# Kernel tuning notes

Measured on AMD Instinct MI355X. Metric: run time of the kernel, lower is better.

Reference implementation:

```python
import jax, jax.numpy as jnp
import numpy as np

B = 256      # graph pairs
N = 256      # nodes per graph (uniform -> padding is a reshape)
DEG = 16     # avg degree
D = 32       # one_hot_dim
F1, F2, F3 = 128, 64, 64
T = 16       # tensor_neurons
BINS = 16
BOT = 16     # bottle_neck_neurons


def setup_inputs() -> dict:
    key = jax.random.key(0)
    ks = jax.random.split(key, 24)
    NT = B * N            # total nodes per side
    NE = B * N * DEG      # total directed edges per side
    x_q = jax.random.normal(ks[0], (NT, D), jnp.float32)
    x_c = jax.random.normal(ks[1], (NT, D), jnp.float32)
    edge_q = jax.random.randint(ks[2], (2, NE), 0, NT, jnp.int32)
    edge_c = jax.random.randint(ks[3], (2, NE), 0, NT, jnp.int32)
    qgraph_sizes = jnp.full((B,), N, jnp.int32)
    cgraph_sizes = jnp.full((B,), N, jnp.int32)

    def glorot(k, shape):
        fan = sum(shape[-2:]) if len(shape) >= 2 else shape[0] * 2
        return jax.random.uniform(k, shape, jnp.float32, -1.0, 1.0) * np.sqrt(6.0 / fan)

    params = dict(
        W1=glorot(ks[4], (D, F1)), b1=jnp.zeros((F1,), jnp.float32),
        W2=glorot(ks[5], (F1, F2)), b2=jnp.zeros((F2,), jnp.float32),
        W3=glorot(ks[6], (F2, F3)), b3=jnp.zeros((F3,), jnp.float32),
        attn_w=glorot(ks[7], (F3, F3)),
        ntn_a_w=glorot(ks[8], (T, F3, F3)),
        ntn_b_w=glorot(ks[9], (2 * F3, T)),
        ntn_bias=glorot(ks[10], (T, 1)),
        fc1_w=glorot(ks[11], (T + BINS, BOT)), fc1_b=jnp.zeros((BOT,), jnp.float32),
        fc2_w=glorot(ks[12], (BOT, 1)), fc2_b=jnp.zeros((1,), jnp.float32),
    )
    return dict(x_q=x_q, edge_q=edge_q, x_c=x_c, edge_c=edge_c,
                qgraph_sizes=qgraph_sizes, cgraph_sizes=cgraph_sizes, **params)


def _gcn(x, src, dst, W, b):
    n = x.shape[0]
    h = x @ W
    loop = jnp.arange(n, dtype=src.dtype)
    s = jnp.concatenate([src, loop])
    d = jnp.concatenate([dst, loop])
    deg = jax.ops.segment_sum(jnp.ones(s.shape, h.dtype), d, num_segments=n)
    dinv = jnp.where(deg > 0, jax.lax.rsqrt(jnp.maximum(deg, 1.0)), 0.0)
    coef = (dinv[s] * dinv[d])[:, None]
    return jax.ops.segment_sum(h[s] * coef, d, num_segments=n) + b


def _gnn(x, ei, W1, b1, W2, b2, W3, b3):
    src, dst = ei[0], ei[1]
    h = jax.nn.relu(_gcn(x, src, dst, W1, b1))        # dropout is identity in eval
    h = jax.nn.relu(_gcn(h, src, dst, W2, b2))
    return _gcn(h, src, dst, W3, b3)                  # [B*N, F3]


def _att_pool(q, attn_w, sizes):
    # q: [B, N, F3]
    ctx = jnp.tanh((q.sum(axis=1) @ attn_w) / sizes.astype(q.dtype)[:, None])  # [B, F3]
    sig = jax.nn.sigmoid(jnp.einsum('bnf,bf->bn', q, ctx))                      # [B, N]
    return jnp.einsum('bnf,bn->bf', q, sig)                                     # [B, F3]


def _pair_hist(q, c):
    # per-pair histogram of q @ c^T with BINS bins over each pair's [min, max]
    s = jax.lax.stop_gradient(jnp.einsum('bnf,bmf->bnm', q, c))  # [B, N, N]
    mn = s.min(axis=(1, 2), keepdims=True)
    mx = s.max(axis=(1, 2), keepdims=True)
    idx = jnp.clip(jnp.floor((s - mn) / jnp.maximum(mx - mn, 1e-12) * BINS),
                   0, BINS - 1).astype(jnp.int32)
    gid = (idx + jnp.arange(B, dtype=jnp.int32)[:, None, None] * BINS).reshape(-1)
    h = jax.ops.segment_sum(jnp.ones(gid.shape, jnp.float32), gid,
                            num_segments=B * BINS).reshape(B, BINS)
    return h / h.sum(axis=1, keepdims=True)


def reference(x_q, edge_q, x_c, edge_c, qgraph_sizes, cgraph_sizes,
              W1, b1, W2, b2, W3, b3, attn_w, ntn_a_w, ntn_b_w, ntn_bias,
              fc1_w, fc1_b, fc2_w, fc2_b):
    q = _gnn(x_q, edge_q, W1, b1, W2, b2, W3, b3).reshape(B, N, F3)
    c = _gnn(x_c, edge_c, W1, b1, W2, b2, W3, b3).reshape(B, N, F3)
    e1 = _att_pool(q, attn_w, qgraph_sizes)
    e2 = _att_pool(c, attn_w, cgraph_sizes)
    ntn = (jnp.einsum('bi,tij,bj->bt', e1, ntn_a_w, e2)
           + jnp.concatenate([e1, e2], axis=-1) @ ntn_b_w
           + ntn_bias[:, 0])
    scores = jax.nn.relu(ntn)                                   # [B, T]
    hist = _pair_hist(q, c)                                     # [B, BINS]
    scores = jnp.concatenate([scores, hist], axis=1)
    scores = jax.nn.relu(scores @ fc1_w + fc1_b)
    p = jax.nn.sigmoid(scores @ fc2_w + fc2_b)[:, 0]            # [B]
    ged = -0.5 * (qgraph_sizes + cgraph_sizes).astype(p.dtype) * jnp.log(p)
    return ged
```

## Files before the change

kernel.cpp:

```cpp
#include <hip/hip_runtime.h>
#include <hip/hip_bf16.h>
#include <math.h>

#define BB 256
#define NN 256
#define NT (BB*NN)
#define NT2 (2*NT)
#define NE (NT*16)
#define DD 32
#define F1C 128
#define F2C 64
#define F3C 64
#define TT 16
#define BINS 16

#define NBUCK 256
#define BSHIFT 9
#define BNODES 512
#define BCAP 10240
#define EPB 4096

typedef __attribute__((ext_vector_type(8))) short short8;
typedef __attribute__((ext_vector_type(4))) float f32x4;
typedef __attribute__((ext_vector_type(2))) float f32x2;

__device__ inline float b2f(ushort u) { return __uint_as_float(((uint)u) << 16); }
__device__ inline ushort f2b(float f) {
    uint u = __float_as_uint(f);
    return (ushort)((u + 0x7fffu + ((u >> 16) & 1u)) >> 16);
}
__device__ inline float clamp8(float v) { return fminf(fmaxf(v, -448.0f), 448.0f); }
__device__ inline uchar f2f8(float v) {
    int r = __builtin_amdgcn_cvt_pk_fp8_f32(clamp8(v), 0.0f, 0, false);
    return (uchar)(r & 0xff);
}
__device__ inline void f8x8_acc(uint2 w, float* acc) {
    f32x2 p;
    p = __builtin_amdgcn_cvt_pk_f32_fp8(w.x, false); acc[0] += p.x; acc[1] += p.y;
    p = __builtin_amdgcn_cvt_pk_f32_fp8(w.x, true);  acc[2] += p.x; acc[3] += p.y;
    p = __builtin_amdgcn_cvt_pk_f32_fp8(w.y, false); acc[4] += p.x; acc[5] += p.y;
    p = __builtin_amdgcn_cvt_pk_f32_fp8(w.y, true);  acc[6] += p.x; acc[7] += p.y;
}
__device__ inline uint2 f8x8_pack(const float* v) {
    uint2 r;
    r.x = (uint)__builtin_amdgcn_cvt_pk_fp8_f32(clamp8(v[0]), clamp8(v[1]), 0, false);
    r.x = (uint)__builtin_amdgcn_cvt_pk_fp8_f32(clamp8(v[2]), clamp8(v[3]), (int)r.x, true);
    r.y = (uint)__builtin_amdgcn_cvt_pk_fp8_f32(clamp8(v[4]), clamp8(v[5]), 0, false);
    r.y = (uint)__builtin_amdgcn_cvt_pk_fp8_f32(clamp8(v[6]), clamp8(v[7]), (int)r.y, true);
    return r;
}

__global__ __launch_bounds__(256) void zero_k(int* __restrict__ gcount) {
    gcount[threadIdx.x] = 0;
}

__global__ __launch_bounds__(256) void csr_p1_k(const int* __restrict__ eq, const int* __restrict__ ec,
                                                uint* __restrict__ staged, int* __restrict__ gcount) {
    __shared__ uint s_pk[EPB];
    __shared__ int s_cnt[NBUCK];
    __shared__ int s_off[NBUCK];
    __shared__ int s_base[NBUCK];
    __shared__ int s_gb[NBUCK];
    int t = threadIdx.x;
    bool sideB = blockIdx.x >= 256;
    const int* edge = sideB ? ec : eq;
    int off = sideB ? NT : 0;
    int e0 = (blockIdx.x & 255) * EPB;
    s_cnt[t] = 0;
    __syncthreads();
    uint pk[16]; int bk[16];
#pragma unroll
    for (int j = 0; j < 16; j++) {
        int e = e0 + j * 256 + t;
        int s = edge[e] + off;
        int d = edge[NE + e] + off;
        bk[j] = d >> BSHIFT;
        pk[j] = ((uint)s << BSHIFT) | (uint)(d & (BNODES - 1));
        atomicAdd(&s_cnt[bk[j]], 1);
    }
    __syncthreads();
    s_off[t] = s_cnt[t];
    __syncthreads();
    for (int o = 1; o < NBUCK; o <<= 1) {
        int x = (t >= o) ? s_off[t - o] : 0;
        __syncthreads();
        s_off[t] += x;
        __syncthreads();
    }
    {
        int ex = s_off[t] - s_cnt[t];
        s_base[t] = ex;
        s_off[t] = ex;
        s_gb[t] = atomicAdd(&gcount[t], s_cnt[t]);
    }
    __syncthreads();
#pragma unroll
    for (int j = 0; j < 16; j++) {
        int pos = atomicAdd(&s_off[bk[j]], 1);
        s_pk[pos] = pk[j];
    }
    __syncthreads();
    int w = t >> 6, l = t & 63;
    int bsel = l >> 4, l16 = l & 15;
    for (int pb = w; pb < NBUCK / 4; pb += 4) {
        int b = pb * 4 + bsel;
        int n = s_cnt[b], st = s_base[b], gb = s_gb[b];
        if (gb + n > BCAP) n = max(0, BCAP - gb);
        for (int i = l16; i < n; i += 16)
            staged[b * BCAP + gb + i] = s_pk[st + i];
    }
}

__global__ __launch_bounds__(256) void csr_p2_k(const uint* __restrict__ staged, const int* __restrict__ gcount,
                                                int* __restrict__ rp, int* __restrict__ indeg,
                                                float* __restrict__ dinv, int* __restrict__ ep) {
    int b = blockIdx.x;
    int t = threadIdx.x;
    __shared__ int cnt[BNODES];
    __shared__ int fl[BNODES];
    __shared__ int wsum[256];
    __shared__ int gsc[NBUCK];
    cnt[t] = 0; cnt[t + 256] = 0;
    gsc[t] = min(gcount[t], BCAP);
    __syncthreads();
    for (int off = 1; off < NBUCK; off <<= 1) {
        int x = (t >= off) ? gsc[t - off] : 0;
        __syncthreads();
        gsc[t] += x;
        __syncthreads();
    }
    int gbase = (b == 0) ? 0 : gsc[b - 1];
    int n = min(gcount[b], BCAP);
    const uint* sb = staged + (size_t)b * BCAP;
    int i = t;
    for (; i + 768 < n; i += 1024) {
        uint p0 = sb[i];
        uint p1 = sb[i + 256];
        uint p2 = sb[i + 512];
        uint p3 = sb[i + 768];
        atomicAdd(&cnt[p0 & (BNODES - 1)], 1);
        atomicAdd(&cnt[p1 & (BNODES - 1)], 1);
        atomicAdd(&cnt[p2 & (BNODES - 1)], 1);
        atomicAdd(&cnt[p3 & (BNODES - 1)], 1);
    }
    for (; i < n; i += 256)
        atomicAdd(&cnt[sb[i] & (BNODES - 1)], 1);
    __syncthreads();
    int base2 = t * 2;
    int c0 = cnt[base2], c1 = cnt[base2 + 1];
    int s2 = c0 + c1;
    wsum[t] = s2;
    __syncthreads();
    for (int off = 1; off < 256; off <<= 1) {
        int x = (t >= off) ? wsum[t - off] : 0;
        __syncthreads();
        wsum[t] += x;
        __syncthreads();
    }
    int p = gbase + wsum[t] - s2;
    int v0 = b * BNODES + base2;
    rp[v0] = p;          fl[base2] = p;
    indeg[v0] = c0;      dinv[v0] = rsqrtf((float)(c0 + 1));
    p += c0;
    rp[v0 + 1] = p;      fl[base2 + 1] = p;
    indeg[v0 + 1] = c1;  dinv[v0 + 1] = rsqrtf((float)(c1 + 1));
    __syncthreads();
    i = t;
    for (; i + 768 < n; i += 1024) {
        uint p0 = sb[i];
        uint p1 = sb[i + 256];
        uint p2 = sb[i + 512];
        uint p3 = sb[i + 768];
        ep[atomicAdd(&fl[p0 & (BNODES - 1)], 1)] = (int)(p0 >> BSHIFT);
        ep[atomicAdd(&fl[p1 & (BNODES - 1)], 1)] = (int)(p1 >> BSHIFT);
        ep[atomicAdd(&fl[p2 & (BNODES - 1)], 1)] = (int)(p2 >> BSHIFT);
        ep[atomicAdd(&fl[p3 & (BNODES - 1)], 1)] = (int)(p3 >> BSHIFT);
    }
    for (; i < n; i += 256) {
        uint pk = sb[i];
        ep[atomicAdd(&fl[pk & (BNODES - 1)], 1)] = (int)(pk >> BSHIFT);
    }
}

__global__ __launch_bounds__(256) void cvt2w_k(const float* __restrict__ a, const float* __restrict__ b,
                                               const float* __restrict__ dinv, ushort* __restrict__ out,
                                               const float* __restrict__ W1, const float* __restrict__ W2,
                                               const float* __restrict__ W3, ushort* __restrict__ Wt1,
                                               ushort* __restrict__ Wt2, uchar* __restrict__ Wt3f8) {
    const int NB_X = NT2 * DD / 4 / 256;
    if (blockIdx.x < NB_X) {
        int i = blockIdx.x * 256 + threadIdx.x;
        const int per = NT * DD / 4;
        bool sideB = i >= per;
        const float4* src = (const float4*)(sideB ? b : a);
        float4 v = src[sideB ? i - per : i];
        float dv = dinv[i / (DD / 4)];
        ushort4 o;
        o.x = f2b(v.x * dv); o.y = f2b(v.y * dv); o.z = f2b(v.z * dv); o.w = f2b(v.w * dv);
        ((ushort4*)out)[i] = o;
    } else {
        int i = (blockIdx.x - NB_X) * 256 + threadIdx.x;
        if (i < DD * F1C)  { int k = i / F1C, n = i % F1C; Wt1[n * DD + k]  = f2b(W1[i]); }
        if (i < F1C * F2C) { int k = i / F2C, n = i % F2C; Wt2[n * F1C + k] = f2b(W2[i]); }
        if (i < F2C * F3C) { int k = i / F3C, n = i % F3C; Wt3f8[n * F2C + k] = f2f8(W3[i]); }
    }
}

template<int F, bool BIAS, bool RELU>
__global__ __launch_bounds__(256) void agg_bf_k(const ushort* __restrict__ in, const int* __restrict__ rp,
                                                const int* __restrict__ indeg, const int* __restrict__ ep,
                                                const float* __restrict__ dinv,
                                                const float* __restrict__ bias, ushort* __restrict__ out) {
    constexpr int LPV = F / 8;
    constexpr int VPB = 256 / LPV;
    int g = threadIdx.x / LPV;
    int l = threadIdx.x % LPV;
    int v = blockIdx.x * VPB + g;
    float dv = dinv[v];
    short8 rs = *(const short8*)(in + (size_t)v * F + l * 8);
    float acc[8];
#pragma unroll
    for (int j = 0; j < 8; j++) acc[j] = b2f((ushort)rs[j]);
    int start = rp[v];
    int cnt   = indeg[v];
    int i = 0;
    for (; i + 4 <= cnt; i += 4) {
        int s0 = ep[start + i];
        int s1 = ep[start + i + 1];
        int s2 = ep[start + i + 2];
        int s3 = ep[start + i + 3];
        short8 r0 = *(const short8*)(in + (size_t)s0 * F + l * 8);
        short8 r1 = *(const short8*)(in + (size_t)s1 * F + l * 8);
        short8 r2 = *(const short8*)(in + (size_t)s2 * F + l * 8);
        short8 r3 = *(const short8*)(in + (size_t)s3 * F + l * 8);
#pragma unroll
        for (int j = 0; j < 8; j++) {
            acc[j] += b2f((ushort)r0[j]);
            acc[j] += b2f((ushort)r1[j]);
            acc[j] += b2f((ushort)r2[j]);
            acc[j] += b2f((ushort)r3[j]);
        }
    }
    for (; i < cnt; i++) {
        int s0 = ep[start + i];
        short8 r0 = *(const short8*)(in + (size_t)s0 * F + l * 8);
#pragma unroll
        for (int j = 0; j < 8; j++) acc[j] += b2f((ushort)r0[j]);
    }
    short8 o;
#pragma unroll
    for (int j = 0; j < 8; j++) {
        float x = dv * acc[j];
        if (BIAS) x += bias[l * 8 + j];
        if (RELU) x = fmaxf(x, 0.0f);
        o[j] = (short)f2b(x);
    }
    *(short8*)(out + (size_t)v * F + l * 8) = o;
}

template<bool OUT_BF16, bool BIAS, bool RELU>
__global__ __launch_bounds__(256) void agg_f8_k(const uchar* __restrict__ in, const int* __restrict__ rp,
                                                const int* __restrict__ indeg, const int* __restrict__ ep,
                                                const float* __restrict__ dinv,
                                                const float* __restrict__ bias, void* __restrict__ outp) {
    int g = threadIdx.x >> 3;
    int l = threadIdx.x & 7;
    int v = blockIdx.x * 32 + g;
    float dv = dinv[v];
    float acc[8] = {0, 0, 0, 0, 0, 0, 0, 0};
    f8x8_acc(*(const uint2*)(in + (size_t)v * 64 + l * 8), acc);
    int start = rp[v];
    int cnt   = indeg[v];
    int i = 0;
    for (; i + 8 <= cnt; i += 8) {
        int sx[8];
#pragma unroll
        for (int j = 0; j < 8; j++) sx[j] = ep[start + i + j];
        uint2 gx[8];
#pragma unroll
        for (int j = 0; j < 8; j++) gx[j] = *(const uint2*)(in + (size_t)sx[j] * 64 + l * 8);
#pragma unroll
        for (int j = 0; j < 8; j++) f8x8_acc(gx[j], acc);
    }
    for (; i + 4 <= cnt; i += 4) {
        int s0 = ep[start + i];
        int s1 = ep[start + i + 1];
        int s2 = ep[start + i + 2];
        int s3 = ep[start + i + 3];
        uint2 g0 = *(const uint2*)(in + (size_t)s0 * 64 + l * 8);
        uint2 g1 = *(const uint2*)(in + (size_t)s1 * 64 + l * 8);
        uint2 g2 = *(const uint2*)(in + (size_t)s2 * 64 + l * 8);
        uint2 g3 = *(const uint2*)(in + (size_t)s3 * 64 + l * 8);
        f8x8_acc(g0, acc); f8x8_acc(g1, acc); f8x8_acc(g2, acc); f8x8_acc(g3, acc);
    }
    for (; i < cnt; i++) {
        int s0 = ep[start + i];
        f8x8_acc(*(const uint2*)(in + (size_t)s0 * 64 + l * 8), acc);
    }
#pragma unroll
    for (int j = 0; j < 8; j++) {
        float x = dv * acc[j];
        if (BIAS) x += bias[l * 8 + j];
        if (RELU) x = fmaxf(x, 0.0f);
        acc[j] = x;
    }
    if (OUT_BF16) {
        short8 o;
#pragma unroll
        for (int j = 0; j < 8; j++) o[j] = (short)f2b(acc[j]);
        *(short8*)((ushort*)outp + (size_t)v * 64 + l * 8) = o;
    } else {
        *(uint2*)((uchar*)outp + (size_t)v * 64 + l * 8) = f8x8_pack(acc);
    }
}

__global__ __launch_bounds__(256) void gemm12_k(const ushort* __restrict__ xa,
                                                const ushort* __restrict__ Wt1,
                                                const float* __restrict__ b1,
                                                const ushort* __restrict__ Wt2,
                                                const float* __restrict__ dinv,
                                                uchar* __restrict__ h8a) {
    __shared__ ushort s_h1[128][136];
    int w = threadIdx.x >> 6, lane = threadIdx.x & 63;
    int r16 = lane & 15, quad = lane >> 4, koff = quad * 8;
    size_t rows0 = (size_t)blockIdx.x * 128;

    short8 af1[2];
#pragma unroll
    for (int mt = 0; mt < 2; mt++)
        af1[mt] = *(const short8*)(xa + (rows0 + (w * 2 + mt) * 16 + r16) * 32 + koff);
#pragma unroll
    for (int nt = 0; nt < 8; nt++) {
        short8 bfr = *(const short8*)(Wt1 + (size_t)(nt * 16 + r16) * 32 + koff);
        f32x4 acc[2] = {{0.f,0.f,0.f,0.f},{0.f,0.f,0.f,0.f}};
        acc[0] = __builtin_amdgcn_mfma_f32_16x16x32_bf16(af1[0], bfr, acc[0], 0, 0, 0);
        acc[1] = __builtin_amdgcn_mfma_f32_16x16x32_bf16(af1[1], bfr, acc[1], 0, 0, 0);
        int col = nt * 16 + r16;
        float bc = b1[col];
#pragma unroll
        for (int mt = 0; mt < 2; mt++)
#pragma unroll
            for (int r = 0; r < 4; r++) {
                int rl = (w * 2 + mt) * 16 + quad * 4 + r;
                s_h1[rl][col] = f2b(fmaxf(acc[mt][r] + bc, 0.0f));
            }
    }
    __syncthreads();

    short8 af2[4][2];
#pragma unroll
    for (int kc = 0; kc < 4; kc++)
#pragma unroll
        for (int mt = 0; mt < 2; mt++)
            af2[kc][mt] = *(const short8*)&s_h1[(w * 2 + mt) * 16 + r16][kc * 32 + koff];
    float dvr[2][4];
#pragma unroll
    for (int mt = 0; mt < 2; mt++)
#pragma unroll
        for (int r = 0; r < 4; r++)
            dvr[mt][r] = dinv[rows0 + (w * 2 + mt) * 16 + quad * 4 + r];
#pragma unroll
    for (int nt = 0; nt < 4; nt++) {
        f32x4 acc[2] = {{0.f,0.f,0.f,0.f},{0.f,0.f,0.f,0.f}};
#pragma unroll
        for (int kc = 0; kc < 4; kc++) {
            short8 bfr = *(const short8*)(Wt2 + (size_t)(nt * 16 + r16) * 128 + kc * 32 + koff);
            acc[0] = __builtin_amdgcn_mfma_f32_16x16x32_bf16(af2[kc][0], bfr, acc[0], 0, 0, 0);
            acc[1] = __builtin_amdgcn_mfma_f32_16x16x32_bf16(af2[kc][1], bfr, acc[1], 0, 0, 0);
        }
#pragma unroll
        for (int mt = 0; mt < 2; mt++)
#pragma unroll
            for (int r = 0; r < 4; r++) {
                size_t row = rows0 + (w * 2 + mt) * 16 + quad * 4 + r;
                int col = nt * 16 + r16;
                h8a[row * 64 + col] = f2f8(acc[mt][r] * dvr[mt][r]);
            }
    }
}

__global__ __launch_bounds__(256) void gemm_f8_k(const uchar* __restrict__ A8,
                                                 const uchar* __restrict__ Wt8,
                                                 const float* __restrict__ dinv,
                                                 uchar* __restrict__ out8) {
    int w = threadIdx.x >> 6, lane = threadIdx.x & 63;
    int r16 = lane & 15, koff = (lane >> 4) * 8;
    size_t rows0 = (size_t)blockIdx.x * 128;

    long af[2][2];
#pragma unroll
    for (int kc = 0; kc < 2; kc++)
#pragma unroll
        for (int mt = 0; mt < 2; mt++)
            af[kc][mt] = *(const long*)(A8 + (rows0 + (w * 2 + mt) * 16 + r16) * 64 + kc * 32 + koff);

    float dvr[2][4];
#pragma unroll
    for (int mt = 0; mt < 2; mt++)
#pragma unroll
        for (int r = 0; r < 4; r++)
            dvr[mt][r] = dinv[rows0 + (w * 2 + mt) * 16 + (lane >> 4) * 4 + r];

#pragma unroll
    for (int nt = 0; nt < 4; nt++) {
        f32x4 acc[2] = {{0.f,0.f,0.f,0.f},{0.f,0.f,0.f,0.f}};
#pragma unroll
        for (int kc = 0; kc < 2; kc++) {
            long b = *(const long*)(Wt8 + (size_t)(nt * 16 + r16) * 64 + kc * 32 + koff);
            acc[0] = __builtin_amdgcn_mfma_f32_16x16x32_fp8_fp8(af[kc][0], b, acc[0], 0, 0, 0);
            acc[1] = __builtin_amdgcn_mfma_f32_16x16x32_fp8_fp8(af[kc][1], b, acc[1], 0, 0, 0);
        }
#pragma unroll
        for (int mt = 0; mt < 2; mt++) {
#pragma unroll
            for (int r = 0; r < 4; r++) {
                size_t row = rows0 + (w * 2 + mt) * 16 + (lane >> 4) * 4 + r;
                int col = nt * 16 + (lane & 15);
                out8[row * 64 + col] = f2f8(acc[mt][r] * dvr[mt][r]);
            }
        }
    }
}

__global__ __launch_bounds__(256) void pool_hist_k(const ushort* __restrict__ fin,
                                                   const int* __restrict__ qsz, const int* __restrict__ csz,
                                                   const float* __restrict__ attn_w,
                                                   float* __restrict__ e_out, float* __restrict__ histp) {
    __shared__ float smemf[17472];
    int t = threadIdx.x;
    if (blockIdx.x < 512) {
        int b = blockIdx.x & 255;
        bool is_c = blockIdx.x >= BB;
        const ushort* emb = fin + (size_t)blockIdx.x * NN * F3C;
        float size = (float)((is_c ? csz : qsz)[b]);
        float* eo = e_out + (is_c ? BB * F3C : 0) + b * F3C;
        float (*s_emb)[F3C + 1] = (float(*)[F3C + 1])smemf;
        float* s_red = smemf + 256 * 65;
        float* s_sq  = s_red + 256;
        float* s_ctx = s_sq + 64;
        float* s_sig = s_ctx + 64;
        int f = t & 63;
        int w = t >> 6;
#pragma unroll
        for (int it = 0; it < 8; it++) {
            int idx = it * 2048 + t * 8;
            int row = idx >> 6, f0 = idx & 63;
            short8 v = *(const short8*)(emb + idx);
#pragma unroll
            for (int j = 0; j < 8; j++) s_emb[row][f0 + j] = b2f((ushort)v[j]);
        }
        __syncthreads();
        float psum = 0.0f;
#pragma unroll 8
        for (int i2 = 0; i2 < 64; i2++) psum += s_emb[w * 64 + i2][f];
        s_red[w * 64 + f] = psum;
        __syncthreads();
        if (w == 0) {
            s_sq[f] = s_red[f] + s_red[64 + f] + s_red[128 + f] + s_red[192 + f];
            float acc = 0.0f;
            for (int k = 0; k < 64; k++) acc += s_sq[k] * attn_w[k * 64 + f];
            s_ctx[f] = tanhf(acc / size);
        }
        __syncthreads();
        {
            float acc = 0.0f;
#pragma unroll 8
            for (int k = 0; k < 64; k++) acc += s_emb[t][k] * s_ctx[k];
            s_sig[t] = 1.0f / (1.0f + expf(-acc));
        }
        __syncthreads();
        float eacc = 0.0f;
#pragma unroll 8
        for (int i = 0; i < 64; i++) {
            int n = w * 64 + i;
            eacc += s_sig[n] * s_emb[n][f];
        }
        s_red[w * 64 + f] = eacc;
        __syncthreads();
        if (w == 0) eo[f] = s_red[f] + s_red[64 + f] + s_red[128 + f] + s_red[192 + f];
    } else {
        int b = blockIdx.x - 512;
        const ushort* qb = fin + (size_t)b * NN * 64;
        const ushort* cb = fin + (size_t)(NT + b * NN) * 64;
        int lane = t & 63;
        int w = t >> 6;
        int r16 = lane & 15, koff = (lane >> 4) * 8;
        ushort (*cb_s)[72] = (ushort(*)[72])smemf;
        int* h = (int*)(smemf + 9216);
        int* hp = h + 16 * 256;
        float* smn = (float*)(hp + 256);
        float* smx = smn + 4;
        float* s_sc = smx + 4;

#pragma unroll
        for (int it = 0; it < 8; it++) {
            int idx = it * 2048 + t * 8;
            int row = idx >> 6, f0 = idx & 63;
            *(short8*)&cb_s[row][f0] = *(const short8*)(cb + idx);
        }
        short8 a[4][2];
#pragma unroll
        for (int i = 0; i < 4; i++) {
            int row = (w * 4 + i) * 16 + r16;
#pragma unroll
            for (int kk = 0; kk < 2; kk++)
                a[i][kk] = *(const short8*)(qb + row * 64 + kk * 32 + koff);
        }
        __syncthreads();
        float mn = 1e30f, mx = -1e30f;
        for (int mt = 0; mt < 16; mt++) {
            int crow = mt * 16 + r16;
            short8 b0 = *(const short8*)&cb_s[crow][koff];
            short8 b1 = *(const short8*)&cb_s[crow][32 + koff];
#pragma unroll
            for (int i = 0; i < 4; i++) {
                f32x4 acc = {0.0f, 0.0f, 0.0f, 0.0f};
                acc = __builtin_amdgcn_mfma_f32_16x16x32_bf16(a[i][0], b0, acc, 0, 0, 0);
                acc = __builtin_amdgcn_mfma_f32_16x16x32_bf16(a[i][1], b1, acc, 0, 0, 0);
                mn = fminf(mn, fminf(fminf(acc[0], acc[1]), fminf(acc[2], acc[3])));
                mx = fmaxf(mx, fmaxf(fmaxf(acc[0], acc[1]), fmaxf(acc[2], acc[3])));
            }
        }
        for (int off = 32; off; off >>= 1) {
            mn = fminf(mn, __shfl_xor(mn, off, 64));
            mx = fmaxf(mx, __shfl_xor(mx, off, 64));
        }
        if (lane == 0) { smn[w] = mn; smx[w] = mx; }
        __syncthreads();
        if (t == 0) {
            float m0 = fminf(fminf(smn[0], smn[1]), fminf(smn[2], smn[3]));
            float m1 = fmaxf(fmaxf(smx[0], smx[1]), fmaxf(smx[2], smx[3]));
            s_sc[0] = m0;
            s_sc[1] = 16.0f / fmaxf(m1 - m0, 1e-12f);
        }
#pragma unroll
        for (int i = 0; i < 16; i++) h[i * 256 + t] = 0;
        __syncthreads();
        float bmn = s_sc[0], bscale = s_sc[1];
        for (int mt = 0; mt < 16; mt++) {
            int crow = mt * 16 + r16;
            short8 b0 = *(const short8*)&cb_s[crow][koff];
            short8 b1 = *(const short8*)&cb_s[crow][32 + koff];
#pragma unroll
            for (int i = 0; i < 4; i++) {
                f32x4 acc = {0.0f, 0.0f, 0.0f, 0.0f};
                acc = __builtin_amdgcn_mfma_f32_16x16x32_bf16(a[i][0], b0, acc, 0, 0, 0);
                acc = __builtin_amdgcn_mfma_f32_16x16x32_bf16(a[i][1], b1, acc, 0, 0, 0);
#pragma unroll
                for (int r = 0; r < 4; r++) {
                    int bin = (int)floorf((acc[r] - bmn) * bscale);
                    bin = min(max(bin, 0), 15);
                    h[bin * 256 + t] += 1;
                }
            }
        }
        __syncthreads();
        int bb = t >> 4, part = t & 15;
        int sum = 0;
#pragma unroll
        for (int j = 0; j < 16; j++) sum += h[bb * 256 + part * 16 + j];
        hp[bb * 16 + part] = sum;
        __syncthreads();
        if (t < 16) {
            int s = 0;
#pragma unroll
            for (int j = 0; j < 16; j++) s += hp[t * 16 + j];
            histp[b * 16 + t] = (float)s;
        }
    }
}

__global__ __launch_bounds__(256) void ntn_final_k(const float* __restrict__ e, const float* __restrict__ A,
                                                   const float* __restrict__ bw, const float* __restrict__ bias,
                                                   const float* __restrict__ histp,
                                                   const float* __restrict__ fc1w, const float* __restrict__ fc1b,
                                                   const float* __restrict__ fc2w, const float* __restrict__ fc2b,
                                                   const int* __restrict__ qsz, const int* __restrict__ csz,
                                                   float* __restrict__ out) {
    int b = blockIdx.x;
    int t = threadIdx.x;
    __shared__ float s_e1[64], s_e2[64];
    __shared__ float s_ntn[16];
    __shared__ float s_s[32];
    __shared__ float s_a[16];
    if (t < 64) s_e1[t] = e[b * 64 + t];
    else if (t < 128) s_e2[t - 64] = e[BB * 64 + b * 64 + (t - 64)];
    if (t < 16) s_ntn[t] = 0.0f;
    __syncthreads();
#pragma unroll
    for (int r = 0; r < 4; r++) {
        int idx = t + r * 256;
        int tt = idx >> 6, i = idx & 63;
        const float* Ar = A + (size_t)idx * 64;
        float acc = 0.0f;
        for (int j = 0; j < 64; j++) acc += Ar[j] * s_e2[j];
        atomicAdd(&s_ntn[tt], s_e1[i] * acc);
    }
    __syncthreads();
    if (t < 16) {
        float acc = s_ntn[t] + bias[t];
        for (int k = 0; k < 64; k++) acc += s_e1[k] * bw[k * 16 + t];
        for (int k = 0; k < 64; k++) acc += s_e2[k] * bw[(64 + k) * 16 + t];
        s_s[t] = fmaxf(acc, 0.0f);
        s_s[16 + t] = histp[b * 16 + t] * (1.0f / 65536.0f);
    }
    __syncthreads();
    if (t < 16) {
        float a = fc1b[t];
        for (int k = 0; k < 32; k++) a += s_s[k] * fc1w[k * 16 + t];
        s_a[t] = fmaxf(a, 0.0f);
    }
    __syncthreads();
    if (t == 0) {
        float z = fc2b[0];
        for (int j = 0; j < 16; j++) z += s_a[j] * fc2w[j];
        float nz = -z;
        float sp = (nz > 20.0f) ? nz : log1pf(expf(nz));
        out[b] = 0.5f * (float)(qsz[b] + csz[b]) * sp;
    }
}

extern "C" void kernel_launch(void* const* d_in, const int* in_sizes, int n_in,
                              void* d_out, int out_size, void* d_ws, size_t ws_size,
                              hipStream_t stream) {
    const float* x_q    = (const float*)d_in[0];
    const int*   edge_q = (const int*)d_in[1];
    const float* x_c    = (const float*)d_in[2];
    const int*   edge_c = (const int*)d_in[3];
    const int*   qsz    = (const int*)d_in[4];
    const int*   csz    = (const int*)d_in[5];
    const float* W1 = (const float*)d_in[6];
    const float* b1 = (const float*)d_in[7];
    const float* W2 = (const float*)d_in[8];
    const float* b2 = (const float*)d_in[9];
    const float* W3 = (const float*)d_in[10];
    const float* b3 = (const float*)d_in[11];
    const float* attn_w  = (const float*)d_in[12];
    const float* ntn_a   = (const float*)d_in[13];
    const float* ntn_b   = (const float*)d_in[14];
    const float* ntn_bias= (const float*)d_in[15];
    const float* fc1w = (const float*)d_in[16];
    const float* fc1b = (const float*)d_in[17];
    const float* fc2w = (const float*)d_in[18];
    const float* fc2b = (const float*)d_in[19];
    float* out = (float*)d_out;

    char* w = (char*)d_ws;
    auto alloc = [&](size_t bytes) -> void* {
        void* p = (void*)w;
        w += (bytes + 255) & ~(size_t)255;
        return p;
    };
    int*    rp     = (int*)alloc((size_t)NT2 * 4);
    int*    indeg  = (int*)alloc((size_t)NT2 * 4);
    float*  dinv   = (float*)alloc((size_t)NT2 * 4);
    int*    gcount = (int*)alloc(NBUCK * 4);
    uint*   staged = (uint*)alloc((size_t)NBUCK * BCAP * 4);
    int*    ep     = (int*)alloc((size_t)2 * NE * 4);
    ushort* xb     = (ushort*)alloc((size_t)NT2 * 32 * 2);
    ushort* xa     = (ushort*)alloc((size_t)NT2 * 32 * 2);
    uchar*  h8a    = (uchar*)alloc((size_t)NT2 * 64);
    uchar*  h8b    = (uchar*)alloc((size_t)NT2 * 64);
    ushort* fin    = (ushort*)alloc((size_t)NT2 * 64 * 2);
    ushort* Wt1    = (ushort*)alloc((size_t)DD * F1C * 2);
    ushort* Wt2    = (ushort*)alloc((size_t)F1C * F2C * 2);
    uchar*  Wt3f8  = (uchar*)alloc((size_t)F2C * F3C);
    float*  e12    = (float*)alloc(2 * BB * 64 * 4);
    float*  histp  = (float*)alloc(256 * 16 * 4);

    zero_k<<<1, 256, 0, stream>>>(gcount);
    csr_p1_k<<<512, 256, 0, stream>>>(edge_q, edge_c, staged, gcount);
    csr_p2_k<<<NBUCK, 256, 0, stream>>>(staged, gcount, rp, indeg, dinv, ep);

    cvt2w_k<<<NT2 * 32 / 4 / 256 + 64, 256, 0, stream>>>(x_q, x_c, dinv, xb,
                                                         W1, W2, W3, Wt1, Wt2, Wt3f8);

    agg_bf_k<32, false, false><<<NT2 / 64, 256, 0, stream>>>(xb, rp, indeg, ep, dinv, nullptr, xa);
    gemm12_k<<<NT2 / 128, 256, 0, stream>>>(xa, Wt1, b1, Wt2, dinv, h8a);
    agg_f8_k<false, true, true><<<NT2 / 32, 256, 0, stream>>>(h8a, rp, indeg, ep, dinv, b2, h8b);
    gemm_f8_k<<<NT2 / 128, 256, 0, stream>>>(h8b, Wt3f8, dinv, h8a);
    agg_f8_k<true, true, false><<<NT2 / 32, 256, 0, stream>>>(h8a, rp, indeg, ep, dinv, b3, fin);

    pool_hist_k<<<768, 256, 0, stream>>>(fin, qsz, csz, attn_w, e12, histp);
    ntn_final_k<<<BB, 256, 0, stream>>>(e12, ntn_a, ntn_b, ntn_bias, histp,
                                        fc1w, fc1b, fc2w, fc2b, qsz, csz, out);
}
```

Baseline: 285.5 us.

## Fuse weight and feature conversion into CSR kernels, widen gather unroll

Moves the weight transpose and conversion into extra blocks of the first CSR pass, and folds the dinv-scaled bf16 conversion of node features into the second CSR pass using degrees kept in shared memory. This removes one kernel launch and one dinv reload. The first aggregation kernel is specialised to width 32 and gains an 8-way unrolled gather. Edge-index loads in all aggregation kernels become nontemporal. The NTN kernel now uses float4 loads and a wavefront shuffle reduction in place of shared-memory atomics.

```diff
diff --git a/kernel.cpp b/kernel.cpp
--- a/kernel.cpp
+++ b/kernel.cpp
@@ -54,72 +54,85 @@
     gcount[threadIdx.x] = 0;
 }
 
-__global__ __launch_bounds__(256) void csr_p1_k(const int* __restrict__ eq, const int* __restrict__ ec,
-                                                uint* __restrict__ staged, int* __restrict__ gcount) {
-    __shared__ uint s_pk[EPB];
-    __shared__ int s_cnt[NBUCK];
-    __shared__ int s_off[NBUCK];
-    __shared__ int s_base[NBUCK];
-    __shared__ int s_gb[NBUCK];
+__global__ __launch_bounds__(256) void p1cvt_k(const int* __restrict__ eq, const int* __restrict__ ec,
+                                               uint* __restrict__ staged, int* __restrict__ gcount,
+                                               const float* __restrict__ W1, const float* __restrict__ W2,
+                                               const float* __restrict__ W3, ushort* __restrict__ Wt1,
+                                               ushort* __restrict__ Wt2, uchar* __restrict__ Wt3f8) {
     int t = threadIdx.x;
-    bool sideB = blockIdx.x >= 256;
-    const int* edge = sideB ? ec : eq;
-    int off = sideB ? NT : 0;
-    int e0 = (blockIdx.x & 255) * EPB;
-    s_cnt[t] = 0;
-    __syncthreads();
-    uint pk[16]; int bk[16];
-#pragma unroll
-    for (int j = 0; j < 16; j++) {
-        int e = e0 + j * 256 + t;
-        int s = edge[e] + off;
-        int d = edge[NE + e] + off;
-        bk[j] = d >> BSHIFT;
-        pk[j] = ((uint)s << BSHIFT) | (uint)(d & (BNODES - 1));
-        atomicAdd(&s_cnt[bk[j]], 1);
-    }
-    __syncthreads();
-    s_off[t] = s_cnt[t];
-    __syncthreads();
-    for (int o = 1; o < NBUCK; o <<= 1) {
-        int x = (t >= o) ? s_off[t - o] : 0;
-        __syncthreads();
-        s_off[t] += x;
-        __syncthreads();
-    }
-    {
-        int ex = s_off[t] - s_cnt[t];
-        s_base[t] = ex;
-        s_off[t] = ex;
-        s_gb[t] = atomicAdd(&gcount[t], s_cnt[t]);
-    }
-    __syncthreads();
-#pragma unroll
-    for (int j = 0; j < 16; j++) {
-        int pos = atomicAdd(&s_off[bk[j]], 1);
-        s_pk[pos] = pk[j];
-    }
-    __syncthreads();
-    int w = t >> 6, l = t & 63;
-    int bsel = l >> 4, l16 = l & 15;
-    for (int pb = w; pb < NBUCK / 4; pb += 4) {
-        int b = pb * 4 + bsel;
-        int n = s_cnt[b], st = s_base[b], gb = s_gb[b];
-        if (gb + n > BCAP) n = max(0, BCAP - gb);
-        for (int i = l16; i < n; i += 16)
-            staged[b * BCAP + gb + i] = s_pk[st + i];
+    if (blockIdx.x < 512) {
+        __shared__ uint s_pk[EPB];
+        __shared__ int s_cnt[NBUCK];
+        __shared__ int s_off[NBUCK];
+        __shared__ int s_base[NBUCK];
+        __shared__ int s_gb[NBUCK];
+        bool sideB = blockIdx.x >= 256;
+        const int* edge = sideB ? ec : eq;
+        int off = sideB ? NT : 0;
+        int e0 = (blockIdx.x & 255) * EPB;
+        s_cnt[t] = 0;
+        __syncthreads();
+        uint pk[16]; int bk[16];
+#pragma unroll
+        for (int j = 0; j < 16; j++) {
+            int e = e0 + j * 256 + t;
+            int s = edge[e] + off;
+            int d = edge[NE + e] + off;
+            bk[j] = d >> BSHIFT;
+            pk[j] = ((uint)s << BSHIFT) | (uint)(d & (BNODES - 1));
+            atomicAdd(&s_cnt[bk[j]], 1);
+        }
+        __syncthreads();
+        s_off[t] = s_cnt[t];
+        __syncthreads();
+        for (int o = 1; o < NBUCK; o <<= 1) {
+            int x = (t >= o) ? s_off[t - o] : 0;
+            __syncthreads();
+            s_off[t] += x;
+            __syncthreads();
+        }
+        {
+            int ex = s_off[t] - s_cnt[t];
+            s_base[t] = ex;
+            s_off[t] = ex;
+            s_gb[t] = atomicAdd(&gcount[t], s_cnt[t]);
+        }
+        __syncthreads();
+#pragma unroll
+        for (int j = 0; j < 16; j++) {
+            int pos = atomicAdd(&s_off[bk[j]], 1);
+            s_pk[pos] = pk[j];
+        }
+        __syncthreads();
+        int w = t >> 6, l = t & 63;
+        int bsel = l >> 4, l16 = l & 15;
+        for (int pb = w; pb < NBUCK / 4; pb += 4) {
+            int bkt = pb * 4 + bsel;
+            int n = s_cnt[bkt], st = s_base[bkt], gb = s_gb[bkt];
+            if (gb + n > BCAP) n = max(0, BCAP - gb);
+            for (int i = l16; i < n; i += 16)
+                staged[bkt * BCAP + gb + i] = s_pk[st + i];
+        }
+    } else {
+        int i = (blockIdx.x - 512) * 256 + t;
+        if (i < DD * F1C)  { int k = i / F1C, n = i % F1C; Wt1[n * DD + k]  = f2b(W1[i]); }
+        if (i < F1C * F2C) { int k = i / F2C, n = i % F2C; Wt2[n * F1C + k] = f2b(W2[i]); }
+        if (i < F2C * F3C) { int k = i / F3C, n = i % F3C; Wt3f8[n * F2C + k] = f2f8(W3[i]); }
     }
 }
 
 __global__ __launch_bounds__(256) void csr_p2_k(const uint* __restrict__ staged, const int* __restrict__ gcount,
                                                 int* __restrict__ rp, int* __restrict__ indeg,
-                                                float* __restrict__ dinv, int* __restrict__ ep) {
+                                                float* __restrict__ dinv, int* __restrict__ ep,
+                                                const float* __restrict__ xq, const float* __restrict__ xc,
+                                                ushort* __restrict__ xb) {
     int b = blockIdx.x;
     int t = threadIdx.x;
     __shared__ int cnt[BNODES];
     __shared__ int fl[BNODES];
     __shared__ int wsum[256];
     __shared__ int gsc[NBUCK];
+    __shared__ float sdv[BNODES];
     cnt[t] = 0; cnt[t + 256] = 0;
     gsc[t] = min(gcount[t], BCAP);
     __syncthreads();
@@ -159,11 +172,13 @@
     }
     int p = gbase + wsum[t] - s2;
     int v0 = b * BNODES + base2;
+    float d0 = rsqrtf((float)(c0 + 1));
+    float d1 = rsqrtf((float)(c1 + 1));
     rp[v0] = p;          fl[base2] = p;
-    indeg[v0] = c0;      dinv[v0] = rsqrtf((float)(c0 + 1));
+    indeg[v0] = c0;      dinv[v0] = d0;      sdv[base2] = d0;
     p += c0;
     rp[v0 + 1] = p;      fl[base2 + 1] = p;
-    indeg[v0 + 1] = c1;  dinv[v0 + 1] = rsqrtf((float)(c1 + 1));
+    indeg[v0 + 1] = c1;  dinv[v0 + 1] = d1;  sdv[base2 + 1] = d1;
     __syncthreads();
     i = t;
     for (; i + 768 < n; i += 1024) {
@@ -180,59 +195,58 @@
         uint pk = sb[i];
         ep[atomicAdd(&fl[pk & (BNODES - 1)], 1)] = (int)(pk >> BSHIFT);
     }
-}
-
-__global__ __launch_bounds__(256) void cvt2w_k(const float* __restrict__ a, const float* __restrict__ b,
-                                               const float* __restrict__ dinv, ushort* __restrict__ out,
-                                               const float* __restrict__ W1, const float* __restrict__ W2,
-                                               const float* __restrict__ W3, ushort* __restrict__ Wt1,
-                                               ushort* __restrict__ Wt2, uchar* __restrict__ Wt3f8) {
-    const int NB_X = NT2 * DD / 4 / 256;
-    if (blockIdx.x < NB_X) {
-        int i = blockIdx.x * 256 + threadIdx.x;
-        const int per = NT * DD / 4;
-        bool sideB = i >= per;
-        const float4* src = (const float4*)(sideB ? b : a);
-        float4 v = src[sideB ? i - per : i];
-        float dv = dinv[i / (DD / 4)];
-        ushort4 o;
-        o.x = f2b(v.x * dv); o.y = f2b(v.y * dv); o.z = f2b(v.z * dv); o.w = f2b(v.w * dv);
-        ((ushort4*)out)[i] = o;
-    } else {
-        int i = (blockIdx.x - NB_X) * 256 + threadIdx.x;
-        if (i < DD * F1C)  { int k = i / F1C, n = i % F1C; Wt1[n * DD + k]  = f2b(W1[i]); }
-        if (i < F1C * F2C) { int k = i / F2C, n = i % F2C; Wt2[n * F1C + k] = f2b(W2[i]); }
-        if (i < F2C * F3C) { int k = i / F3C, n = i % F3C; Wt3f8[n * F2C + k] = f2f8(W3[i]); }
-    }
-}
-
-template<int F, bool BIAS, bool RELU>
+    {
+        const float* xs = (b < 128) ? (xq + (size_t)b * BNODES * DD)
+                                    : (xc + ((size_t)b * BNODES - NT) * DD);
+        ushort* xd = xb + (size_t)b * BNODES * DD;
+        for (int g = t; g < BNODES * DD / 4; g += 256) {
+            int r = g >> 3;
+            float4 v = ((const float4*)xs)[g];
+            float dv = sdv[r];
+            ushort4 o;
+            o.x = f2b(v.x * dv); o.y = f2b(v.y * dv);
+            o.z = f2b(v.z * dv); o.w = f2b(v.w * dv);
+            ((ushort4*)xd)[g] = o;
+        }
+    }
+}
+
 __global__ __launch_bounds__(256) void agg_bf_k(const ushort* __restrict__ in, const int* __restrict__ rp,
                                                 const int* __restrict__ indeg, const int* __restrict__ ep,
                                                 const float* __restrict__ dinv,
-                                                const float* __restrict__ bias, ushort* __restrict__ out) {
-    constexpr int LPV = F / 8;
-    constexpr int VPB = 256 / LPV;
-    int g = threadIdx.x / LPV;
-    int l = threadIdx.x % LPV;
-    int v = blockIdx.x * VPB + g;
+                                                ushort* __restrict__ out) {
+    int g = threadIdx.x >> 2;
+    int l = threadIdx.x & 3;
+    int v = blockIdx.x * 64 + g;
     float dv = dinv[v];
-    short8 rs = *(const short8*)(in + (size_t)v * F + l * 8);
+    short8 rs = *(const short8*)(in + (size_t)v * 32 + l * 8);
     float acc[8];
 #pragma unroll
     for (int j = 0; j < 8; j++) acc[j] = b2f((ushort)rs[j]);
     int start = rp[v];
     int cnt   = indeg[v];
     int i = 0;
+    for (; i + 8 <= cnt; i += 8) {
+        int sx[8];
+#pragma unroll
+        for (int j = 0; j < 8; j++) sx[j] = __builtin_nontemporal_load(ep + start + i + j);
+        short8 r[8];
+#pragma unroll
+        for (int j = 0; j < 8; j++) r[j] = *(const short8*)(in + (size_t)sx[j] * 32 + l * 8);
+#pragma unroll
+        for (int j = 0; j < 8; j++)
+#pragma unroll
+            for (int k = 0; k < 8; k++) acc[k] += b2f((ushort)r[j][k]);
+    }
     for (; i + 4 <= cnt; i += 4) {
-        int s0 = ep[start + i];
-        int s1 = ep[start + i + 1];
-        int s2 = ep[start + i + 2];
-        int s3 = ep[start + i + 3];
-        short8 r0 = *(const short8*)(in + (size_t)s0 * F + l * 8);
-        short8 r1 = *(const short8*)(in + (size_t)s1 * F + l * 8);
-        short8 r2 = *(const short8*)(in + (size_t)s2 * F + l * 8);
-        short8 r3 = *(const short8*)(in + (size_t)s3 * F + l * 8);
+        int s0 = __builtin_nontemporal_load(ep + start + i);
+        int s1 = __builtin_nontemporal_load(ep + start + i + 1);
+        int s2 = __builtin_nontemporal_load(ep + start + i + 2);
+        int s3 = __builtin_nontemporal_load(ep + start + i + 3);
+        short8 r0 = *(const short8*)(in + (size_t)s0 * 32 + l * 8);
+        short8 r1 = *(const short8*)(in + (size_t)s1 * 32 + l * 8);
+        short8 r2 = *(const short8*)(in + (size_t)s2 * 32 + l * 8);
+        short8 r3 = *(const short8*)(in + (size_t)s3 * 32 + l * 8);
 #pragma unroll
         for (int j = 0; j < 8; j++) {
             acc[j] += b2f((ushort)r0[j]);
@@ -242,20 +256,15 @@
         }
     }
     for (; i < cnt; i++) {
-        int s0 = ep[start + i];
-        short8 r0 = *(const short8*)(in + (size_t)s0 * F + l * 8);
+        int s0 = __builtin_nontemporal_load(ep + start + i);
+        short8 r0 = *(const short8*)(in + (size_t)s0 * 32 + l * 8);
 #pragma unroll
         for (int j = 0; j < 8; j++) acc[j] += b2f((ushort)r0[j]);
     }
     short8 o;
 #pragma unroll
-    for (int j = 0; j < 8; j++) {
-        float x = dv * acc[j];
-        if (BIAS) x += bias[l * 8 + j];
-        if (RELU) x = fmaxf(x, 0.0f);
-        o[j] = (short)f2b(x);
-    }
-    *(short8*)(out + (size_t)v * F + l * 8) = o;
+    for (int j = 0; j < 8; j++) o[j] = (short)f2b(dv * acc[j]);
+    *(short8*)(out + (size_t)v * 32 + l * 8) = o;
 }
 
 template<bool OUT_BF16, bool BIAS, bool RELU>
@@ -275,7 +284,7 @@
     for (; i + 8 <= cnt; i += 8) {
         int sx[8];
 #pragma unroll
-        for (int j = 0; j < 8; j++) sx[j] = ep[start + i + j];
+        for (int j = 0; j < 8; j++) sx[j] = __builtin_nontemporal_load(ep + start + i + j);
         uint2 gx[8];
 #pragma unroll
         for (int j = 0; j < 8; j++) gx[j] = *(const uint2*)(in + (size_t)sx[j] * 64 + l * 8);
@@ -283,10 +292,10 @@
         for (int j = 0; j < 8; j++) f8x8_acc(gx[j], acc);
     }
     for (; i + 4 <= cnt; i += 4) {
-        int s0 = ep[start + i];
-        int s1 = ep[start + i + 1];
-        int s2 = ep[start + i + 2];
-        int s3 = ep[start + i + 3];
+        int s0 = __builtin_nontemporal_load(ep + start + i);
+        int s1 = __builtin_nontemporal_load(ep + start + i + 1);
+        int s2 = __builtin_nontemporal_load(ep + start + i + 2);
+        int s3 = __builtin_nontemporal_load(ep + start + i + 3);
         uint2 g0 = *(const uint2*)(in + (size_t)s0 * 64 + l * 8);
         uint2 g1 = *(const uint2*)(in + (size_t)s1 * 64 + l * 8);
         uint2 g2 = *(const uint2*)(in + (size_t)s2 * 64 + l * 8);
@@ -294,7 +303,7 @@
         f8x8_acc(g0, acc); f8x8_acc(g1, acc); f8x8_acc(g2, acc); f8x8_acc(g3, acc);
     }
     for (; i < cnt; i++) {
-        int s0 = ep[start + i];
+        int s0 = __builtin_nontemporal_load(ep + start + i);
         f8x8_acc(*(const uint2*)(in + (size_t)s0 * 64 + l * 8), acc);
     }
 #pragma unroll
@@ -579,22 +588,28 @@
                                                    float* __restrict__ out) {
     int b = blockIdx.x;
     int t = threadIdx.x;
+    int lane = t & 63, w = t >> 6;
     __shared__ float s_e1[64], s_e2[64];
     __shared__ float s_ntn[16];
     __shared__ float s_s[32];
     __shared__ float s_a[16];
     if (t < 64) s_e1[t] = e[b * 64 + t];
     else if (t < 128) s_e2[t - 64] = e[BB * 64 + b * 64 + (t - 64)];
-    if (t < 16) s_ntn[t] = 0.0f;
     __syncthreads();
 #pragma unroll
     for (int r = 0; r < 4; r++) {
         int idx = t + r * 256;
-        int tt = idx >> 6, i = idx & 63;
-        const float* Ar = A + (size_t)idx * 64;
+        const float4* Ar = (const float4*)(A + (size_t)idx * 64);
         float acc = 0.0f;
-        for (int j = 0; j < 64; j++) acc += Ar[j] * s_e2[j];
-        atomicAdd(&s_ntn[tt], s_e1[i] * acc);
+#pragma unroll
+        for (int j = 0; j < 16; j++) {
+            float4 a4 = Ar[j];
+            acc += a4.x * s_e2[4 * j] + a4.y * s_e2[4 * j + 1]
+                 + a4.z * s_e2[4 * j + 2] + a4.w * s_e2[4 * j + 3];
+        }
+        float p = s_e1[lane] * acc;
+        for (int off = 32; off; off >>= 1) p += __shfl_xor(p, off, 64);
+        if (lane == 0) s_ntn[w + 4 * r] = p;
     }
     __syncthreads();
     if (t < 16) {
@@ -669,13 +684,12 @@
     float*  histp  = (float*)alloc(256 * 16 * 4);
 
     zero_k<<<1, 256, 0, stream>>>(gcount);
-    csr_p1_k<<<512, 256, 0, stream>>>(edge_q, edge_c, staged, gcount);
-    csr_p2_k<<<NBUCK, 256, 0, stream>>>(staged, gcount, rp, indeg, dinv, ep);
-
-    cvt2w_k<<<NT2 * 32 / 4 / 256 + 64, 256, 0, stream>>>(x_q, x_c, dinv, xb,
-                                                         W1, W2, W3, Wt1, Wt2, Wt3f8);
-
-    agg_bf_k<32, false, false><<<NT2 / 64, 256, 0, stream>>>(xb, rp, indeg, ep, dinv, nullptr, xa);
+    p1cvt_k<<<512 + 32, 256, 0, stream>>>(edge_q, edge_c, staged, gcount,
+                                          W1, W2, W3, Wt1, Wt2, Wt3f8);
+    csr_p2_k<<<NBUCK, 256, 0, stream>>>(staged, gcount, rp, indeg, dinv, ep,
+                                        x_q, x_c, xb);
+
+    agg_bf_k<<<NT2 / 64, 256, 0, stream>>>(xb, rp, indeg, ep, dinv, xa);
     gemm12_k<<<NT2 / 128, 256, 0, stream>>>(xa, Wt1, b1, Wt2, dinv, h8a);
     agg_f8_k<false, true, true><<<NT2 / 32, 256, 0, stream>>>(h8a, rp, indeg, ep, dinv, b2, h8b);
     gemm_f8_k<<<NT2 / 128, 256, 0, stream>>>(h8b, Wt3f8, dinv, h8a);
```

Measured after the change: 300.2 us. 1.05x slower.
